# Kernel tuning notes

Hardware: AMD Instinct MI355X
Metric: run time of the kernel (lower is better)

## Reference

```python
import jax, jax.numpy as jnp
import numpy as np

B, C, H, W = 4, 64, 64, 64
RATIO = 8  # channel reduction in the channel-attention branch
C8 = C // RATIO


def conv1x1(x, Wt, b):
    # 1x1 conv == channel-mixing matmul. Wt: (out_c, in_c), x: (B, in_c, H, W)
    return jnp.einsum('oc,bchw->bohw', Wt, x) + b[None, :, None, None]


def setup_inputs() -> dict:
    key = jax.random.key(0)
    ks = jax.random.split(key, 12)
    s = 0.02
    return {
        'x': jax.random.normal(ks[0], (B, C, H, W), dtype=jnp.float32),
        'y': jax.random.normal(ks[1], (B, C, H, W), dtype=jnp.float32),
        'Wq': jax.random.normal(ks[2], (C, C), dtype=jnp.float32) * s,
        'bq': jnp.zeros((C,), dtype=jnp.float32),
        'Wk': jax.random.normal(ks[3], (C, C), dtype=jnp.float32) * s,
        'bk': jnp.zeros((C,), dtype=jnp.float32),
        'Wv': jax.random.normal(ks[4], (C, C), dtype=jnp.float32) * s,
        'bv': jnp.zeros((C,), dtype=jnp.float32),
        'Wq1': jax.random.normal(ks[5], (C8, C), dtype=jnp.float32) * s,
        'bq1': jnp.zeros((C8,), dtype=jnp.float32),
        'Wk1': jax.random.normal(ks[6], (C8, C), dtype=jnp.float32) * s,
        'bk1': jnp.zeros((C8,), dtype=jnp.float32),
    }


def reference(x, y, Wq, bq, Wk, bk, Wv, bv, Wq1, bq1, Wk1, bk1):
    b, c, h, w = x.shape
    hw = h * w
    # cross-attention branch: query from y, key/value from x
    Q = conv1x1(y, Wq, bq).reshape(b, c, hw)   # (B, C, HW)
    K = conv1x1(x, Wk, bk).reshape(b, c, hw)
    V = conv1x1(x, Wv, bv).reshape(b, c, hw)
    attn = jax.nn.softmax(jnp.einsum('bcq,bck->bqk', Q, K), axis=-1)  # (B, HW, HW)
    # channel-attention branch (PAM-style spatial map from x, ratio 8)
    Q1 = conv1x1(x, Wq1, bq1).reshape(b, C8, hw)
    K1 = conv1x1(x, Wk1, bk1).reshape(b, C8, hw)
    attn1 = jax.nn.softmax(jnp.einsum('bcq,bck->bqk', Q1, K1), axis=-1)  # (B, HW, HW)
    # out = attn @ V^T + attn1 @ V^T, shape (B, HW, C)
    out = jnp.einsum('bqk,bck->bqc', attn, V) + jnp.einsum('bqk,bck->bqc', attn1, V)
    return out.transpose(0, 2, 1).reshape(b, c, h, w)
```

## Files before the change

### kernel.cpp

```cpp
#include <hip/hip_runtime.h>
#include <hip/hip_bf16.h>


typedef __bf16 bf16x8 __attribute__((ext_vector_type(8)));
typedef float f32x16 __attribute__((ext_vector_type(16)));

#define MFMA32(A, B, C) __builtin_amdgcn_mfma_f32_32x32x16_bf16((A), (B), (C), 0, 0, 0)

#define LOG2E 1.4426950408889634f
#define EXP2F(x) __builtin_amdgcn_exp2f(x)

__device__ __forceinline__ uint4 ld16(const unsigned short* p) {
  return *reinterpret_cast<const uint4*>(p);
}
__device__ __forceinline__ bf16x8 asbf(uint4 v) {
  return __builtin_bit_cast(bf16x8, v);
}
__device__ __forceinline__ unsigned short f2bf(float f) {
  return __builtin_bit_cast(unsigned short, __float2bfloat16(f));
}
__device__ __forceinline__ unsigned pk2(float a, float b) {
  return (unsigned)f2bf(a) | ((unsigned)f2bf(b) << 16);
}

__global__ __launch_bounds__(256) void proj_kernel(
    const float* __restrict__ x, const float* __restrict__ y,
    const float* __restrict__ Wq, const float* __restrict__ bq,
    const float* __restrict__ Wk, const float* __restrict__ bk,
    const float* __restrict__ Wv, const float* __restrict__ bv,
    const float* __restrict__ Wq1, const float* __restrict__ bq1,
    const float* __restrict__ Wk1, const float* __restrict__ bk1,
    unsigned short* __restrict__ Qb, unsigned short* __restrict__ Kb,
    unsigned short* __restrict__ VtT, unsigned short* __restrict__ Q1c,
    unsigned short* __restrict__ K1c)
{
  __shared__ float ldsT[64][64];
  __shared__ float ldsW[64][65];
  __shared__ float ldsW2[64][65];
  __shared__ float ldsW1[8][64];
  __shared__ float ldsW1b[8][64];

  const int t = threadIdx.x;
  const int b = blockIdx.x >> 6;
  const int p0 = (blockIdx.x & 63) << 6;
  const int lane = t & 63;
  const int w = t >> 6;

  for (int i = t; i < 4096; i += 256) {
    int c = i >> 6, p = i & 63;
    ldsT[c][p] = y[(size_t)(b * 64 + c) * 4096 + p0 + p];
    ldsW[c][p] = Wq[i];
    ldsW2[c][p] = Wv[i];
  }
  for (int i = t; i < 512; i += 256) {
    ldsW1[i >> 6][i & 63] = Wq1[i];
    ldsW1b[i >> 6][i & 63] = Wk1[i];
  }
  __syncthreads();

  {
    float acc[16];
    float bias = bq[lane];
#pragma unroll
    for (int pp = 0; pp < 16; ++pp) acc[pp] = bias;
    for (int ic = 0; ic < 64; ++ic) {
      float wv_ = ldsW[lane][ic];
#pragma unroll
      for (int pp = 0; pp < 16; ++pp)
        acc[pp] = fmaf(wv_, ldsT[ic][w * 16 + pp], acc[pp]);
    }
#pragma unroll
    for (int pp = 0; pp < 16; ++pp)
      Qb[(size_t)(b * 4096 + p0 + w * 16 + pp) * 64 + lane] = f2bf(acc[pp] * LOG2E);
  }
  __syncthreads();

  for (int i = t; i < 4096; i += 256) {
    int c = i >> 6, p = i & 63;
    ldsT[c][p] = x[(size_t)(b * 64 + c) * 4096 + p0 + p];
    ldsW[c][p] = Wk[i];
  }
  __syncthreads();

  {
    float acc[16];
    float bias = bk[lane];
#pragma unroll
    for (int pp = 0; pp < 16; ++pp) acc[pp] = bias;
    for (int ic = 0; ic < 64; ++ic) {
      float wv_ = ldsW[lane][ic];
#pragma unroll
      for (int pp = 0; pp < 16; ++pp)
        acc[pp] = fmaf(wv_, ldsT[ic][w * 16 + pp], acc[pp]);
    }
#pragma unroll
    for (int pp = 0; pp < 16; ++pp)
      Kb[(size_t)(b * 4096 + p0 + w * 16 + pp) * 64 + lane] = f2bf(acc[pp]);
  }

  {
    float acc[16];
#pragma unroll
    for (int j = 0; j < 16; ++j) acc[j] = bv[16 * w + j];
    for (int ic = 0; ic < 64; ++ic) {
      float xv = ldsT[ic][lane];
#pragma unroll
      for (int j = 0; j < 16; ++j)
        acc[j] = fmaf(ldsW2[16 * w + j][ic], xv, acc[j]);
    }
    const int k = p0 + lane;
    const int kblk = k >> 5, ki = k & 31;
#pragma unroll
    for (int j = 0; j < 16; ++j)
      VtT[((size_t)(b * 128 + kblk) * 64 + 16 * w + j) * 32 + ki] = f2bf(acc[j]);
  }

  if (w == 0) {
    float acc[8];
#pragma unroll
    for (int j = 0; j < 8; ++j) acc[j] = bq1[j];
    for (int ic = 0; ic < 64; ++ic) {
      float xv = ldsT[ic][lane];
#pragma unroll
      for (int j = 0; j < 8; ++j)
        acc[j] = fmaf(ldsW1[j][ic], xv, acc[j]);
    }
    uint4 o;
    o.x = pk2(acc[0] * LOG2E, acc[1] * LOG2E);
    o.y = pk2(acc[2] * LOG2E, acc[3] * LOG2E);
    o.z = pk2(acc[4] * LOG2E, acc[5] * LOG2E);
    o.w = pk2(acc[6] * LOG2E, acc[7] * LOG2E);
    *reinterpret_cast<uint4*>(Q1c + (size_t)(b * 4096 + p0 + lane) * 8) = o;
  } else if (w == 1) {
    float acc[8];
#pragma unroll
    for (int j = 0; j < 8; ++j) acc[j] = bk1[j];
    for (int ic = 0; ic < 64; ++ic) {
      float xv = ldsT[ic][lane];
#pragma unroll
      for (int j = 0; j < 8; ++j)
        acc[j] = fmaf(ldsW1b[j][ic], xv, acc[j]);
    }
    uint4 o;
    o.x = pk2(acc[0], acc[1]); o.y = pk2(acc[2], acc[3]);
    o.z = pk2(acc[4], acc[5]); o.w = pk2(acc[6], acc[7]);
    *reinterpret_cast<uint4*>(K1c + (size_t)(b * 4096 + p0 + lane) * 8) = o;
  }
}

__global__ __launch_bounds__(512, 2) void attn_kernel(
    const unsigned short* __restrict__ Qb, const unsigned short* __restrict__ Kb,
    const unsigned short* __restrict__ VtT, const unsigned short* __restrict__ Q1c,
    const unsigned short* __restrict__ K1c, float* __restrict__ out)
{
  __shared__ float accbuf[2][2][64][32];
  __shared__ float zbuf[8][2][32];

  const int id = blockIdx.x;
  const int b = (id & 7) >> 1;
  const int qt = (id >> 3) + ((id & 1) << 6);
  const int q0 = qt * 32;

  const int wid = threadIdx.x >> 6;
  const int l = threadIdx.x & 63;
  const int qc = l & 31;
  const int h = l >> 5;

  const int kBeg = wid << 9;
  const int kEnd = kBeg + 512;

  const f32x16 zero16 = {0.f,0.f,0.f,0.f, 0.f,0.f,0.f,0.f,
                         0.f,0.f,0.f,0.f, 0.f,0.f,0.f,0.f};
  const uint4 zu4 = {0u, 0u, 0u, 0u};

  const unsigned short* qrow = Qb + (size_t)(b * 4096 + q0 + qc) * 64 + 8 * h;
  bf16x8 qf[4];
#pragma unroll
  for (int m = 0; m < 4; ++m) qf[m] = asbf(ld16(qrow + 16 * m));
  bf16x8 q1f;
  {
    uint4 v = zu4;
    if (h == 0) v = ld16(Q1c + (size_t)(b * 4096 + q0 + qc) * 8);
    q1f = asbf(v);
  }

  f32x16 accA0 = zero16, accA1 = zero16, accB0 = zero16, accB1 = zero16;
  float zA = 0.f, zB = 0.f;

#pragma unroll 1
  for (int k0 = kBeg; k0 < kEnd; k0 += 32) {
    uint4 kf[4], vf[4], k1f;
    {
      const unsigned short* kp = Kb + ((size_t)(b * 4096 + k0 + qc) << 6) + 8 * h;
      kf[0] = ld16(kp);
      kf[1] = ld16(kp + 16);
      kf[2] = ld16(kp + 32);
      kf[3] = ld16(kp + 48);
      k1f = zu4;
      if (h == 0) k1f = ld16(K1c + (size_t)(b * 4096 + k0 + qc) * 8);
      const unsigned short* vp =
          VtT + (((size_t)(b * 128 + (k0 >> 5)) * 64 + qc) << 5) + 8 * h;
      vf[0] = ld16(vp);
      vf[1] = ld16(vp + 16);
      vf[2] = ld16(vp + 32 * 32);
      vf[3] = ld16(vp + 32 * 32 + 16);
    }

    f32x16 sD = MFMA32(asbf(kf[0]), qf[0], zero16);
    sD = MFMA32(asbf(kf[1]), qf[1], sD);
    sD = MFMA32(asbf(kf[2]), qf[2], sD);
    sD = MFMA32(asbf(kf[3]), qf[3], sD);
    f32x16 uD = MFMA32(asbf(k1f), q1f, zero16);

#pragma unroll
    for (int r = 0; r < 16; ++r) { sD[r] = EXP2F(sD[r]); uD[r] = EXP2F(uD[r]); }
    zA += (((sD[0]+sD[1])+(sD[2]+sD[3])) + ((sD[4]+sD[5])+(sD[6]+sD[7]))) +
          (((sD[8]+sD[9])+(sD[10]+sD[11])) + ((sD[12]+sD[13])+(sD[14]+sD[15])));
    zB += (((uD[0]+uD[1])+(uD[2]+uD[3])) + ((uD[4]+uD[5])+(uD[6]+uD[7]))) +
          (((uD[8]+uD[9])+(uD[10]+uD[11])) + ((uD[12]+uD[13])+(uD[14]+uD[15])));

#pragma unroll
    for (int m = 0; m < 2; ++m) {
      unsigned W0 = pk2(sD[8*m+0], sD[8*m+1]);
      unsigned W1 = pk2(sD[8*m+2], sD[8*m+3]);
      unsigned W2 = pk2(sD[8*m+4], sD[8*m+5]);
      unsigned W3 = pk2(sD[8*m+6], sD[8*m+7]);
      auto s1 = __builtin_amdgcn_permlane32_swap((int)W0, (int)W2, false, false);
      auto s2 = __builtin_amdgcn_permlane32_swap((int)W1, (int)W3, false, false);
      uint4 pw;
      pw.x = (unsigned)s1[0]; pw.y = (unsigned)s2[0];
      pw.z = (unsigned)s1[1]; pw.w = (unsigned)s2[1];
      bf16x8 pf = asbf(pw);

      unsigned X0 = pk2(uD[8*m+0], uD[8*m+1]);
      unsigned X1 = pk2(uD[8*m+2], uD[8*m+3]);
      unsigned X2 = pk2(uD[8*m+4], uD[8*m+5]);
      unsigned X3 = pk2(uD[8*m+6], uD[8*m+7]);
      auto t1 = __builtin_amdgcn_permlane32_swap((int)X0, (int)X2, false, false);
      auto t2 = __builtin_amdgcn_permlane32_swap((int)X1, (int)X3, false, false);
      uint4 pw1;
      pw1.x = (unsigned)t1[0]; pw1.y = (unsigned)t2[0];
      pw1.z = (unsigned)t1[1]; pw1.w = (unsigned)t2[1];
      bf16x8 pf1 = asbf(pw1);

      accA0 = MFMA32(asbf(vf[m]),     pf,  accA0);
      accA1 = MFMA32(asbf(vf[2 + m]), pf,  accA1);
      accB0 = MFMA32(asbf(vf[m]),     pf1, accB0);
      accB1 = MFMA32(asbf(vf[2 + m]), pf1, accB1);
    }
  }

  zA += __shfl_xor(zA, 32);
  zB += __shfl_xor(zB, 32);
  if (h == 0) { zbuf[wid][0][qc] = zA; zbuf[wid][1][qc] = zB; }

  auto payload_write = [&](int slot) {
#pragma unroll
    for (int r = 0; r < 16; ++r) {
      const int c0 = (r & 3) + 8 * (r >> 2) + 4 * h;
      accbuf[slot][0][c0][qc]      = accA0[r];
      accbuf[slot][0][c0 + 32][qc] = accA1[r];
      accbuf[slot][1][c0][qc]      = accB0[r];
      accbuf[slot][1][c0 + 32][qc] = accB1[r];
    }
  };
  auto payload_add = [&](int slot) {
#pragma unroll
    for (int r = 0; r < 16; ++r) {
      const int c0 = (r & 3) + 8 * (r >> 2) + 4 * h;
      accA0[r] += accbuf[slot][0][c0][qc];
      accA1[r] += accbuf[slot][0][c0 + 32][qc];
      accB0[r] += accbuf[slot][1][c0][qc];
      accB1[r] += accbuf[slot][1][c0 + 32][qc];
    }
  };

  if (wid == 1) payload_write(0);
  if (wid == 5) payload_write(1);
  __syncthreads();
  if (wid == 0) payload_add(0);
  if (wid == 4) payload_add(1);
  __syncthreads();
  if (wid == 3) payload_write(0);
  if (wid == 7) payload_write(1);
  __syncthreads();
  if (wid == 2) payload_add(0);
  if (wid == 6) payload_add(1);
  __syncthreads();
  if (wid == 2) payload_write(0);
  if (wid == 6) payload_write(1);
  __syncthreads();
  if (wid == 0) payload_add(0);
  if (wid == 4) payload_add(1);
  __syncthreads();
  if (wid == 4) payload_write(0);
  __syncthreads();
  if (wid == 0) {
    payload_add(0);
    float zAt = 0.f, zBt = 0.f;
#pragma unroll
    for (int ww = 0; ww < 8; ++ww) { zAt += zbuf[ww][0][qc]; zBt += zbuf[ww][1][qc]; }
    const float rA = 1.0f / zAt, rB = 1.0f / zBt;
    float* op = out + (size_t)b * (64 * 4096) + q0 + qc;
#pragma unroll
    for (int r = 0; r < 16; ++r) {
      const int c0 = (r & 3) + 8 * (r >> 2) + 4 * h;
      op[(size_t)c0 * 4096]        = accA0[r] * rA + accB0[r] * rB;
      op[(size_t)(c0 + 32) * 4096] = accA1[r] * rA + accB1[r] * rB;
    }
  }
}

extern "C" void kernel_launch(void* const* d_in, const int* in_sizes, int n_in,
                              void* d_out, int out_size, void* d_ws, size_t ws_size,
                              hipStream_t stream) {
  (void)in_sizes; (void)n_in; (void)out_size; (void)ws_size;
  const float* x = (const float*)d_in[0];
  const float* y = (const float*)d_in[1];
  const float* Wq = (const float*)d_in[2];
  const float* bq = (const float*)d_in[3];
  const float* Wk = (const float*)d_in[4];
  const float* bk = (const float*)d_in[5];
  const float* Wv = (const float*)d_in[6];
  const float* bv = (const float*)d_in[7];
  const float* Wq1 = (const float*)d_in[8];
  const float* bq1 = (const float*)d_in[9];
  const float* Wk1 = (const float*)d_in[10];
  const float* bk1 = (const float*)d_in[11];

  char* ws = (char*)d_ws;
  unsigned short* Qb = (unsigned short*)(ws);
  unsigned short* Kb = (unsigned short*)(ws + (2u << 20));
  unsigned short* VtT = (unsigned short*)(ws + (4u << 20));
  unsigned short* Q1c = (unsigned short*)(ws + (6u << 20));
  unsigned short* K1c = (unsigned short*)(ws + (6u << 20) + (256u << 10));

  proj_kernel<<<256, 256, 0, stream>>>(x, y, Wq, bq, Wk, bk, Wv, bv,
                                       Wq1, bq1, Wk1, bk1, Qb, Kb, VtT, Q1c, K1c);
  attn_kernel<<<512, 512, 0, stream>>>(Qb, Kb, VtT, Q1c, K1c, (float*)d_out);
}
```

Baseline: 82.73 us.

## Software-pipeline QK MFMA one tile ahead of softmax/PV in attention loop

Restructures the key loop into a two-stage software pipeline. The QK^T score MFMAs for the next 32-key tile are issued before the exp/pack/PV work of the current tile, so matrix-core and transcendental work can overlap and load latency is hidden. Launch bounds are relaxed from 2 to 1 blocks per CU to give room for the extra live score and K registers, which may lower occupancy.

```diff
diff --git a/kernel.cpp b/kernel.cpp
--- a/kernel.cpp
+++ b/kernel.cpp
@@ -148,7 +148,7 @@
   }
 }
 
-__global__ __launch_bounds__(512, 2) void attn_kernel(
+__global__ __launch_bounds__(512, 1) void attn_kernel(
     const unsigned short* __restrict__ Qb, const unsigned short* __restrict__ Kb,
     const unsigned short* __restrict__ VtT, const unsigned short* __restrict__ Q1c,
     const unsigned short* __restrict__ K1c, float* __restrict__ out)
@@ -167,7 +167,6 @@
   const int h = l >> 5;
 
   const int kBeg = wid << 9;
-  const int kEnd = kBeg + 512;
 
   const f32x16 zero16 = {0.f,0.f,0.f,0.f, 0.f,0.f,0.f,0.f,
                          0.f,0.f,0.f,0.f, 0.f,0.f,0.f,0.f};
@@ -187,30 +186,33 @@
   f32x16 accA0 = zero16, accA1 = zero16, accB0 = zero16, accB1 = zero16;
   float zA = 0.f, zB = 0.f;
 
-#pragma unroll 1
-  for (int k0 = kBeg; k0 < kEnd; k0 += 32) {
-    uint4 kf[4], vf[4], k1f;
-    {
-      const unsigned short* kp = Kb + ((size_t)(b * 4096 + k0 + qc) << 6) + 8 * h;
-      kf[0] = ld16(kp);
-      kf[1] = ld16(kp + 16);
-      kf[2] = ld16(kp + 32);
-      kf[3] = ld16(kp + 48);
-      k1f = zu4;
-      if (h == 0) k1f = ld16(K1c + (size_t)(b * 4096 + k0 + qc) * 8);
-      const unsigned short* vp =
-          VtT + (((size_t)(b * 128 + (k0 >> 5)) * 64 + qc) << 5) + 8 * h;
-      vf[0] = ld16(vp);
-      vf[1] = ld16(vp + 16);
-      vf[2] = ld16(vp + 32 * 32);
-      vf[3] = ld16(vp + 32 * 32 + 16);
-    }
-
-    f32x16 sD = MFMA32(asbf(kf[0]), qf[0], zero16);
-    sD = MFMA32(asbf(kf[1]), qf[1], sD);
-    sD = MFMA32(asbf(kf[2]), qf[2], sD);
-    sD = MFMA32(asbf(kf[3]), qf[3], sD);
-    f32x16 uD = MFMA32(asbf(k1f), q1f, zero16);
+  auto load_k = [&](int k0, uint4* kf, uint4& k1f) {
+    const unsigned short* kp = Kb + ((size_t)(b * 4096 + k0 + qc) << 6) + 8 * h;
+    kf[0] = ld16(kp);
+    kf[1] = ld16(kp + 16);
+    kf[2] = ld16(kp + 32);
+    kf[3] = ld16(kp + 48);
+    k1f = zu4;
+    if (h == 0) k1f = ld16(K1c + (size_t)(b * 4096 + k0 + qc) * 8);
+  };
+
+  auto qk = [&](const uint4* kf, uint4 k1f, f32x16& sD, f32x16& uD) {
+    f32x16 s = MFMA32(asbf(kf[0]), qf[0], zero16);
+    s = MFMA32(asbf(kf[1]), qf[1], s);
+    s = MFMA32(asbf(kf[2]), qf[2], s);
+    s = MFMA32(asbf(kf[3]), qf[3], s);
+    sD = s;
+    uD = MFMA32(asbf(k1f), q1f, zero16);
+  };
+
+  auto finish = [&](int k0, f32x16& sD, f32x16& uD) {
+    uint4 vf[4];
+    const unsigned short* vp =
+        VtT + (((size_t)(b * 128 + (k0 >> 5)) * 64 + qc) << 5) + 8 * h;
+    vf[0] = ld16(vp);
+    vf[1] = ld16(vp + 16);
+    vf[2] = ld16(vp + 32 * 32);
+    vf[3] = ld16(vp + 32 * 32 + 16);
 
 #pragma unroll
     for (int r = 0; r < 16; ++r) { sD[r] = EXP2F(sD[r]); uD[r] = EXP2F(uD[r]); }
@@ -248,6 +250,25 @@
       accB0 = MFMA32(asbf(vf[m]),     pf1, accB0);
       accB1 = MFMA32(asbf(vf[2 + m]), pf1, accB1);
     }
+  };
+
+  uint4 kfA[4], kfB[4], k1fA, k1fB;
+  f32x16 sDA, uDA, sDB, uDB;
+
+  load_k(kBeg, kfA, k1fA);
+  qk(kfA, k1fA, sDA, uDA);
+
+#pragma unroll 1
+  for (int p = 0; p < 8; ++p) {
+    const int k0 = kBeg + (p << 6);
+    load_k(k0 + 32, kfB, k1fB);
+    qk(kfB, k1fB, sDB, uDB);
+    finish(k0, sDA, uDA);
+    if (p < 7) {
+      load_k(k0 + 64, kfA, k1fA);
+      qk(kfA, k1fA, sDA, uDA);
+    }
+    finish(k0 + 32, sDB, uDB);
   }
 
   zA += __shfl_xor(zA, 32);
```

Result: no change. 82.98 us (+0.3%).
